# Kernel optimization log

Measured on AMD Instinct MI355X. Metric: run time of the kernel, lower is better.

The kernel has to match this reference:

```python
import math
import jax, jax.numpy as jnp
import numpy as np

BN_EPS = 1e-5

def _lrelu(x, s):
    return jnp.where(x >= 0, x, s * x)

def _bn(x, g, b):
    # BatchNorm2d in train mode (torch default): biased batch stats over (B,H,W)
    mu = jnp.mean(x, axis=(0, 2, 3), keepdims=True)
    var = jnp.mean((x - mu) ** 2, axis=(0, 2, 3), keepdims=True)
    return (x - mu) / jnp.sqrt(var + BN_EPS) * g[None, :, None, None] + b[None, :, None, None]

def _knn(x, x2, k):
    # x: [B,d,P], x2: [B,d,S] -> idx [B,k,S]: k nearest points of x for each column of x2
    inner = -2.0 * jnp.einsum('bdp,bds->bps', x, x2)
    xx = jnp.sum(x ** 2, axis=1)[:, :, None]    # [B,P,1]
    xx2 = jnp.sum(x2 ** 2, axis=1)[:, None, :]  # [B,1,S]
    d = -xx - inner - xx2                        # [B,P,S], larger = closer
    _, idx = jax.lax.top_k(jnp.transpose(d, (0, 2, 1)), k)  # [B,S,k]
    return jnp.transpose(idx, (0, 2, 1))         # [B,k,S]

def _gather_nb(X, idx, s, k):
    # faithful to torch gether_neibour, including its flat-reshape layout
    B, C, P = X.shape
    base = jnp.arange(B)[:, None, None] * P
    flat = (idx + base).reshape(-1)
    Xt = jnp.transpose(X, (0, 2, 1)).reshape(B * P, C)
    return Xt[flat].reshape(B, s, k, C)

def _c2d(x, W, b):
    return jnp.einsum('oc,bcpk->bopk', W, x) + b[None, :, None, None]

def _c1d(x, W, b):
    return jnp.einsum('oc,bcp->bop', W, x) + b[None, :, None]

def _forward(x, W_pos, b_pos, g2, be2, W_conv, b_conv, g1, be1, W_a1, b_a1, W_a2, b_a2, W_b1, b_b1, W_b2, b_b2, num_points):
    B, C, P = x.shape
    k = 8
    s = num_points
    # ---- Dynamic_sampling_M: uniform mesh over (x,y) bbox, snap to nearest event ----
    L = int(math.ceil(math.sqrt(s)))
    m = jnp.arange(L, dtype=x.dtype) / L
    m01 = jnp.tile(m[None, :], (L, 1)).reshape(1, 1, L * L)
    m02 = jnp.tile(m[:, None], (1, L)).reshape(1, 1, L * L)
    mesh = jnp.broadcast_to(jnp.concatenate([m01, m02], axis=1), (B, 2, L * L))
    Px = jax.lax.stop_gradient(x[:, :2, :])  # knn runs under torch.no_grad
    mn = Px.min(axis=2, keepdims=True)
    mx = Px.max(axis=2, keepdims=True)
    PS = mesh * (mx - mn) + mn
    idx0 = _knn(Px, PS, 1)                                   # [B,1,L*L]
    sp = _gather_nb(x, idx0, L * L, 1)[:, :, 0, :].transpose(0, 2, 1)  # [B,C,s]
    idx = _knn(jax.lax.stop_gradient(x[:, :3, :]), jax.lax.stop_gradient(sp[:, :3, :]), k)  # [B,k,s]
    x1 = jnp.transpose(_gather_nb(x, idx, s, k), (0, 3, 1, 2))  # [B,C,s,k]
    # ---- positional encoding ----
    PA = x1[:, :3, :, :]
    PC = x1[:, :3, :, 0:1]
    diff = PA - PC
    sq = jnp.sum(diff ** 2, axis=1, keepdims=True)
    temp = jnp.where(sq > 0, jnp.sqrt(jnp.where(sq > 0, sq, 1.0)), 0.0)
    PEmb = jnp.concatenate([PA, jnp.broadcast_to(PC, PA.shape), diff, temp], axis=1)  # [B,10,s,k]
    PEmb = _lrelu(_bn(_c2d(PEmb, W_pos, b_pos), g2, be2), 0.2)
    x_ = _lrelu(_bn(_c2d(x1[:, :4, :, :], W_conv, b_conv), g1, be1), 0.2)
    feat = jnp.concatenate([x_, PEmb], axis=1)  # [B,64,s,k]
    att = _c2d(_lrelu(_c2d(feat, W_a1, b_a1), 0.2), W_a2, b_a2)  # [B,1,s,k]
    att = jax.nn.softmax(att, axis=-1)
    feat = jnp.sum(feat * att, axis=-1)  # [B,64,s]
    Fea1 = _c1d(feat, W_b1, b_b1)
    Fea2 = _c1d(x1[:, :4, :, 0], W_b2, b_b2)
    out = _lrelu(Fea1 + Fea2, 0.01)
    return jnp.concatenate([x1[:, :5, :, 0], out], axis=1)  # [B,69,s]

def setup_inputs() -> dict:
    key = jax.random.key(0)
    ks = jax.random.split(key, 8)
    B, C, P = 2, 5, 16384
    num_points = 4096  # perfect square required by the mesh sampler
    outc, inc, h = 64, 4, 32
    w = lambda k_, shape: jax.random.normal(k_, shape, jnp.float32) * 0.05
    x = jax.random.normal(ks[0], (B, C, P), jnp.float32)
    return dict(
        x=x,
        W_pos=w(ks[1], (h, 10)), b_pos=jnp.zeros((h,), jnp.float32),
        g2=jnp.ones((h,), jnp.float32), be2=jnp.zeros((h,), jnp.float32),
        W_conv=w(ks[2], (h, inc)), b_conv=jnp.zeros((h,), jnp.float32),
        g1=jnp.ones((h,), jnp.float32), be1=jnp.zeros((h,), jnp.float32),
        W_a1=w(ks[3], (32, outc)), b_a1=jnp.zeros((32,), jnp.float32),
        W_a2=w(ks[4], (1, 32)), b_a2=jnp.zeros((1,), jnp.float32),
        W_b1=w(ks[5], (outc, outc)), b_b1=jnp.zeros((outc,), jnp.float32),
        W_b2=w(ks[6], (outc, inc)), b_b2=jnp.zeros((outc,), jnp.float32),
        num_points=num_points,
    )

def reference(x, W_pos, b_pos, g2, be2, W_conv, b_conv, g1, be1, W_a1, b_a1, W_a2, b_a2, W_b1, b_b1, W_b2, b_b2, num_points):
    return _forward(x, W_pos, b_pos, g2, be2, W_conv, b_conv, g1, be1, W_a1, b_a1, W_a2, b_a2, W_b1, b_b1, W_b2, b_b2, num_points)
```

## Files before the change

kernel.cpp:

```cpp
#include <hip/hip_runtime.h>
#include <math.h>

#define B_ 2
#define P_ 16384
#define C_ 5
#define S_ 4096
#define KNN_ 8
#define L_ 64

typedef unsigned short u16;
typedef unsigned int u32;

__device__ int   g_f32x, g_f32w;
__device__ float g_mnmx[16];
__device__ int   g_idxk[B_ * KNN_ * S_];
__device__ float g_partials[256 * 128];
__device__ float g_stats[128];

__device__ __forceinline__ float bf2f(u16 u) {
  union { u32 i; float f; } c; c.i = ((u32)u) << 16; return c.f;
}
__device__ __forceinline__ u16 f2bf(float f) {
  union { float f; u32 i; } c; c.f = f;
  u32 r = c.i + 0x7fffu + ((c.i >> 16) & 1u);
  return (u16)(r >> 16);
}
__device__ __forceinline__ float ldany(const void* p, int i, int f32) {
  return f32 ? ((const float*)p)[i] : bf2f(((const u16*)p)[i]);
}

__device__ __forceinline__ double packkey(float d, int idx) {
  u32 bits = __float_as_uint(d);
  u32 key = bits ^ ((u32)(((int)bits) >> 31) | 0x80000000u);
  int hi = (int)(0x3FF00000u | (key >> 12));
  int lo = (int)((key << 20) | ((u32)(16383 - idx) << 6));
  return __hiloint2double(hi, lo);
}
__device__ __forceinline__ int keyidx(double w) {
  return 16383 - (int)(((u32)__double2loint(w) >> 6) & 16383u);
}
__device__ __forceinline__ void ins8(double* t, double v) {
  double m = v;
#pragma unroll
  for (int k = 0; k < 8; ++k) {
    double mn = fmin(t[k], m);
    t[k] = fmax(t[k], m);
    m = mn;
  }
}

__device__ __forceinline__ int chk_bad(const void* p, int n, int tid) {
  int bad = 0;
  for (int i = tid; i < n; i += 256) {
    float f = bf2f(((const u16*)p)[i]);
    if (!(f == f) || fabsf(f) > 1024.0f) bad = 1;
  }
  return bad;
}
__global__ __launch_bounds__(256) void k_prep(const void* x, const void* wpos,
                                              const void* wconv, const void* wa1,
                                              const void* wa2, const void* wb1,
                                              const void* wb2) {
  int tid = threadIdx.x;
  if (blockIdx.x == 0) {
    __shared__ int sx, sw;
    if (tid == 0) { sx = 0; sw = 0; }
    __syncthreads();
    int bx = chk_bad(x, 1024, tid);
    int bw = chk_bad(wpos, 320, tid) | chk_bad(wconv, 128, tid) | chk_bad(wa1, 2048, tid)
           | chk_bad(wa2, 32, tid)   | chk_bad(wb1, 4096, tid)  | chk_bad(wb2, 256, tid);
    if (bx) atomicOr(&sx, 1);
    if (bw) atomicOr(&sw, 1);
    __syncthreads();
    if (tid == 0) { g_f32x = sx; g_f32w = sw; }
    return;
  }
  __shared__ int sbad;
  if (tid == 0) sbad = 0;
  __syncthreads();
  if (chk_bad(x, 1024, tid)) atomicOr(&sbad, 1);
  __syncthreads();
  int f32 = sbad;
  int bc = blockIdx.x - 1;
  int b = bc >> 1, ch = bc & 1;
  int base = (b * C_ + ch) * P_;
  float mn = INFINITY, mx = -INFINITY;
  for (int p = tid; p < P_; p += 256) {
    float v = ldany(x, base + p, f32);
    mn = fminf(mn, v); mx = fmaxf(mx, v);
  }
  for (int off = 32; off; off >>= 1) {
    mn = fminf(mn, __shfl_down(mn, off));
    mx = fmaxf(mx, __shfl_down(mx, off));
  }
  __shared__ float smn[4], smx[4];
  int wid = tid >> 6;
  if ((tid & 63) == 0) { smn[wid] = mn; smx[wid] = mx; }
  __syncthreads();
  if (tid == 0) {
    for (int w = 1; w < 4; ++w) { mn = fminf(mn, smn[w]); mx = fmaxf(mx, smx[w]); }
    g_mnmx[bc * 2] = mn; g_mnmx[bc * 2 + 1] = mx;
  }
}

__global__ __launch_bounds__(256, 6) void k_knn(const void* __restrict__ xv) {
  __shared__ float4 s4[1024];
  __shared__ int sidx[8];
  const int f32 = g_f32x;
  int tid = threadIdx.x;
  int l = tid & 63, g = tid >> 6;
  int sg0 = blockIdx.x * 8 + g * 2;
  int b = sg0 >> 12;
  int base0 = b * C_ * P_, base1 = base0 + P_, base2 = base1 + P_;

  float mn0 = g_mnmx[(b * 2 + 0) * 2], mx0 = g_mnmx[(b * 2 + 0) * 2 + 1];
  float mn1 = g_mnmx[(b * 2 + 1) * 2], mx1 = g_mnmx[(b * 2 + 1) * 2 + 1];
  float ps0[2], ps1[2], xx2[2], best[2]; int bestp[2];
#pragma unroll
  for (int qq = 0; qq < 2; ++qq) {
    int s = (sg0 + qq) & (S_ - 1);
    float mm0 = (float)(s & (L_ - 1)) * 0.015625f;
    float mm1 = (float)(s >> 6) * 0.015625f;
    ps0[qq] = __fadd_rn(__fmul_rn(mm0, __fsub_rn(mx0, mn0)), mn0);
    ps1[qq] = __fadd_rn(__fmul_rn(mm1, __fsub_rn(mx1, mn1)), mn1);
    xx2[qq] = __fadd_rn(__fmul_rn(ps0[qq], ps0[qq]), __fmul_rn(ps1[qq], ps1[qq]));
    best[qq] = -INFINITY; bestp[qq] = 0x7fffffff;
  }
  for (int c = 0; c < 16; ++c) {
    __syncthreads();
    for (int i = tid; i < 1024; i += 256) {
      int gi = c * 1024 + i;
      float a0 = ldany(xv, base0 + gi, f32);
      float a1 = ldany(xv, base1 + gi, f32);
      float xx = __fadd_rn(__fmul_rn(a0, a0), __fmul_rn(a1, a1));
      s4[i] = make_float4(a0, a1, xx, 0.0f);
    }
    __syncthreads();
    for (int t = 0; t < 16; ++t) {
      float4 v = s4[t * 64 + l];
      int ix = c * 1024 + t * 64 + l;
#pragma unroll
      for (int qq = 0; qq < 2; ++qq) {
        float dot = __fadd_rn(__fmul_rn(v.x, ps0[qq]), __fmul_rn(v.y, ps1[qq]));
        float inner = __fmul_rn(-2.0f, dot);
        float d = __fsub_rn(__fsub_rn(-v.z, inner), xx2[qq]);
        bool gt = d > best[qq];
        best[qq] = gt ? d : best[qq];
        bestp[qq] = gt ? ix : bestp[qq];
      }
    }
  }
#pragma unroll
  for (int qq = 0; qq < 2; ++qq) {
    float v = best[qq]; int ix = bestp[qq];
    for (int m = 1; m < 64; m <<= 1) {
      float ov = __shfl_xor(v, m, 64); int op = __shfl_xor(ix, m, 64);
      if (ov > v || (ov == v && op < ix)) { v = ov; ix = op; }
    }
    if (l == 0) sidx[g * 2 + qq] = ix;
  }
  __syncthreads();

  float q0[2], q1[2], q2[2], xx3q[2];
  double t8[2][8];
#pragma unroll
  for (int qq = 0; qq < 2; ++qq) {
    int qi = sidx[g * 2 + qq] & (P_ - 1);
    q0[qq] = ldany(xv, base0 + qi, f32);
    q1[qq] = ldany(xv, base1 + qi, f32);
    q2[qq] = ldany(xv, base2 + qi, f32);
    xx3q[qq] = __fadd_rn(__fadd_rn(__fmul_rn(q0[qq], q0[qq]), __fmul_rn(q1[qq], q1[qq])),
                         __fmul_rn(q2[qq], q2[qq]));
#pragma unroll
    for (int k = 0; k < 8; ++k) t8[qq][k] = -1.0;
  }
  for (int c = 0; c < 16; ++c) {
    __syncthreads();
    for (int i = tid; i < 1024; i += 256) {
      int gi = c * 1024 + i;
      float a0 = ldany(xv, base0 + gi, f32);
      float a1 = ldany(xv, base1 + gi, f32);
      float a2 = ldany(xv, base2 + gi, f32);
      float xx = __fadd_rn(__fadd_rn(__fmul_rn(a0, a0), __fmul_rn(a1, a1)), __fmul_rn(a2, a2));
      s4[i] = make_float4(a0, a1, a2, xx);
    }
    __syncthreads();
    for (int t = 0; t < 16; ++t) {
      float4 v = s4[t * 64 + l];
      int ix = c * 1024 + t * 64 + l;
#pragma unroll
      for (int qq = 0; qq < 2; ++qq) {
        float dot = __fadd_rn(__fadd_rn(__fmul_rn(v.x, q0[qq]), __fmul_rn(v.y, q1[qq])),
                              __fmul_rn(v.z, q2[qq]));
        float inner = __fmul_rn(-2.0f, dot);
        float d = __fsub_rn(__fsub_rn(-v.w, inner), xx3q[qq]);
        ins8(t8[qq], packkey(d, ix));
      }
    }
  }
  double wk[2] = {0.0, 0.0};
#pragma unroll
  for (int qq = 0; qq < 2; ++qq) {
#pragma unroll
    for (int r = 0; r < 8; ++r) {
      double w = t8[qq][0];
      for (int m = 1; m < 64; m <<= 1) w = fmax(w, __shfl_xor(w, m, 64));
      if (l == r) wk[qq] = w;
      bool cns = (t8[qq][0] == w);
#pragma unroll
      for (int k = 0; k < 7; ++k) t8[qq][k] = cns ? t8[qq][k + 1] : t8[qq][k];
      t8[qq][7] = cns ? -1.0 : t8[qq][7];
    }
  }
  if (l < 8) {
#pragma unroll
    for (int qq = 0; qq < 2; ++qq) {
      int s = (sg0 + qq) & (S_ - 1);
      g_idxk[b * 32768 + l * 4096 + s] = keyidx(wk[qq]);
    }
  }
}

__device__ __forceinline__ void elem_vals(const void* xv, int xf32, int xbase,
                                          const int* fb, int n,
                                          const float* sWpos, const float* sbpos,
                                          const float* sWconv, const float* sbconv,
                                          float* val ) {
  int p = fb[n] & (P_ - 1);
  int p0 = fb[n & ~7] & (P_ - 1);
  float xvv[4];
#pragma unroll
  for (int c = 0; c < 4; ++c) xvv[c] = ldany(xv, xbase + c * P_ + p, xf32);
  float pc[3];
#pragma unroll
  for (int c = 0; c < 3; ++c) pc[c] = ldany(xv, xbase + c * P_ + p0, xf32);
  float d0 = xvv[0] - pc[0], d1 = xvv[1] - pc[1], d2 = xvv[2] - pc[2];
  float sq = d0 * d0 + d1 * d1 + d2 * d2;
  float temp = (sq > 0.0f) ? sqrtf(sq) : 0.0f;
  float pe[10] = {xvv[0], xvv[1], xvv[2], pc[0], pc[1], pc[2], d0, d1, d2, temp};
#pragma unroll
  for (int o = 0; o < 32; ++o) {
    float acc = sbconv[o];
#pragma unroll
    for (int c = 0; c < 4; ++c) acc = fmaf(sWconv[o * 4 + c], xvv[c], acc);
    val[o] = acc;
  }
#pragma unroll
  for (int o = 0; o < 32; ++o) {
    float acc = sbpos[o];
#pragma unroll
    for (int c = 0; c < 10; ++c) acc = fmaf(sWpos[o * 10 + c], pe[c], acc);
    val[32 + o] = acc;
  }
}

__global__ __launch_bounds__(256) void k_partial(const void* __restrict__ x,
                                                 const void* __restrict__ Wpos,
                                                 const void* __restrict__ bpos,
                                                 const void* __restrict__ Wconv,
                                                 const void* __restrict__ bconv) {
  __shared__ float sWpos[320], sbpos[32], sWconv[128], sbconv[32];
  __shared__ float sacc[4][128];
  int tid = threadIdx.x;
  int xf32 = g_f32x, wf32 = g_f32w;
  for (int i2 = tid; i2 < 320; i2 += 256) sWpos[i2] = ldany(Wpos, i2, wf32);
  if (tid < 128) sWconv[tid] = ldany(Wconv, tid, wf32);
  if (tid < 32) { sbpos[tid] = ldany(bpos, tid, wf32); sbconv[tid] = ldany(bconv, tid, wf32); }
  __syncthreads();
  int t = blockIdx.x * 256 + tid;
  int b = t >> 15, n = t & 32767;
  const int* fb = g_idxk + b * 32768;
  float val[64];
  elem_vals(x, xf32, b * C_ * P_, fb, n, sWpos, sbpos, sWconv, sbconv, val);
  int wid = tid >> 6, lane = tid & 63;
#pragma unroll
  for (int c = 0; c < 64; ++c) {
    float s = val[c], q = val[c] * val[c];
    for (int off = 32; off; off >>= 1) {
      s += __shfl_down(s, off);
      q += __shfl_down(q, off);
    }
    if (lane == 0) { sacc[wid][c * 2] = s; sacc[wid][c * 2 + 1] = q; }
  }
  __syncthreads();
  if (tid < 128) {
    g_partials[blockIdx.x * 128 + tid] =
        sacc[0][tid] + sacc[1][tid] + sacc[2][tid] + sacc[3][tid];
  }
}

__global__ void k_finalize(const void* __restrict__ g1, const void* __restrict__ be1,
                           const void* __restrict__ g2, const void* __restrict__ be2) {
  int ch = threadIdx.x;
  if (ch >= 64) return;
  int wf32 = g_f32w;
  float sum = 0.f, sq = 0.f;
  for (int blk = 0; blk < 256; ++blk) {
    sum += g_partials[blk * 128 + ch * 2];
    sq  += g_partials[blk * 128 + ch * 2 + 1];
  }
  float mean = sum * (1.0f / 65536.0f);
  float var = sq * (1.0f / 65536.0f) - mean * mean;
  int o = ch & 31;
  float g  = ldany(ch < 32 ? g1 : g2, o, wf32);
  float be = ldany(ch < 32 ? be1 : be2, o, wf32);
  float scale = g / sqrtf(var + 1e-5f);
  g_stats[ch * 2] = scale;
  g_stats[ch * 2 + 1] = be - mean * scale;
}

__global__ __launch_bounds__(256) void k_pass2(const void* __restrict__ x,
                                               const void* __restrict__ Wpos,
                                               const void* __restrict__ bpos,
                                               const void* __restrict__ Wconv,
                                               const void* __restrict__ bconv,
                                               const void* __restrict__ Wa1,
                                               const void* __restrict__ ba1,
                                               const void* __restrict__ Wa2,
                                               const void* __restrict__ ba2,
                                               const void* __restrict__ Wb1,
                                               const void* __restrict__ bb1,
                                               const void* __restrict__ Wb2,
                                               const void* __restrict__ bb2,
                                               void* __restrict__ out) {
  __shared__ float sWpos[320], sbpos[32], sWconv[128], sbconv[32];
  __shared__ float sWa1[2048], sba1[32], sWa2[32];
  __shared__ float sWb1[64 * 65];
  __shared__ float sbb1[64], sWb2[256], sbb2[64], sstats[128];
  __shared__ float sba2;
  int tid = threadIdx.x;
  int xf32 = g_f32x, wf32 = g_f32w;
  for (int i2 = tid; i2 < 320; i2 += 256) sWpos[i2] = ldany(Wpos, i2, wf32);
  if (tid < 128) sWconv[tid] = ldany(Wconv, tid, wf32);
  if (tid < 32) { sbpos[tid] = ldany(bpos, tid, wf32); sbconv[tid] = ldany(bconv, tid, wf32); }
  for (int i2 = tid; i2 < 2048; i2 += 256) sWa1[i2] = ldany(Wa1, i2, wf32);
  for (int i2 = tid; i2 < 4096; i2 += 256) sWb1[(i2 >> 6) * 65 + (i2 & 63)] = ldany(Wb1, i2, wf32);
  if (tid >= 32 && tid < 64) { sba1[tid - 32] = ldany(ba1, tid - 32, wf32); sWa2[tid - 32] = ldany(Wa2, tid - 32, wf32); }
  if (tid >= 64 && tid < 128) { sbb1[tid - 64] = ldany(bb1, tid - 64, wf32); sbb2[tid - 64] = ldany(bb2, tid - 64, wf32); }
  if (tid >= 128 && tid < 256) sstats[tid - 128] = g_stats[tid - 128];
  sWb2[tid] = ldany(Wb2, tid, wf32);
  if (tid == 0) sba2 = ldany(ba2, 0, wf32);
  __syncthreads();
  int g = blockIdx.x * 32 + (tid >> 3);
  int j = tid & 7;
  int b = g >> 12, i = g & (S_ - 1);
  int n = i * 8 + j;
  const int* fb = g_idxk + b * 32768;
  int xbase = b * C_ * P_;
  float feat[64];
  elem_vals(x, xf32, xbase, fb, n, sWpos, sbpos, sWconv, sbconv, feat);
#pragma unroll
  for (int c = 0; c < 64; ++c) {
    float v = fmaf(feat[c], sstats[c * 2], sstats[c * 2 + 1]);
    feat[c] = (v >= 0.f) ? v : 0.2f * v;
  }
  float att = sba2;
  for (int h = 0; h < 32; ++h) {
    float acc = sba1[h];
#pragma unroll
    for (int c = 0; c < 64; ++c) acc = fmaf(sWa1[h * 64 + c], feat[c], acc);
    acc = (acc >= 0.f) ? acc : 0.2f * acc;
    att = fmaf(sWa2[h], acc, att);
  }
  float mxv = att;
  for (int mk = 1; mk < 8; mk <<= 1) mxv = fmaxf(mxv, __shfl_xor(mxv, mk, 8));
  float e = expf(att - mxv);
  float se = e;
  for (int mk = 1; mk < 8; mk <<= 1) se += __shfl_xor(se, mk, 8);
  float a = e / se;
#pragma unroll
  for (int c = 0; c < 64; ++c) {
    float w = feat[c] * a;
    w += __shfl_xor(w, 1, 8);
    w += __shfl_xor(w, 2, 8);
    w += __shfl_xor(w, 4, 8);
    feat[c] = w;
  }
  int p0 = fb[i * 8] & (P_ - 1);
  float xc0 = ldany(x, xbase + p0, xf32);
  float xc1 = ldany(x, xbase + P_ + p0, xf32);
  float xc2 = ldany(x, xbase + 2 * P_ + p0, xf32);
  float xc3 = ldany(x, xbase + 3 * P_ + p0, xf32);
  int obase = b * 69 * S_;
#pragma unroll
  for (int oc = 0; oc < 8; ++oc) {
    int o = j * 8 + oc;
    float acc = sbb1[o];
#pragma unroll
    for (int c = 0; c < 64; ++c) acc = fmaf(sWb1[o * 65 + c], feat[c], acc);
    float acc2 = sbb2[o];
    acc2 = fmaf(sWb2[o * 4 + 0], xc0, acc2);
    acc2 = fmaf(sWb2[o * 4 + 1], xc1, acc2);
    acc2 = fmaf(sWb2[o * 4 + 2], xc2, acc2);
    acc2 = fmaf(sWb2[o * 4 + 3], xc3, acc2);
    float r = acc + acc2;
    r = (r >= 0.f) ? r : 0.01f * r;
    int oi = obase + (5 + o) * S_ + i;
    if (xf32) ((float*)out)[oi] = r; else ((u16*)out)[oi] = f2bf(r);
  }
  if (j == 0) {
#pragma unroll
    for (int c = 0; c < 5; ++c) {
      int oi = obase + c * S_ + i;
      if (xf32) ((float*)out)[oi] = ((const float*)x)[xbase + c * P_ + p0];
      else      ((u16*)out)[oi]   = ((const u16*)x)[xbase + c * P_ + p0];
    }
  }
}

extern "C" void kernel_launch(void* const* d_in, const int* in_sizes, int n_in,
                              void* d_out, int out_size, void* d_ws, size_t ws_size,
                              hipStream_t stream) {
  const void* x     = d_in[0];
  const void* Wpos  = d_in[1];
  const void* bpos  = d_in[2];
  const void* g2    = d_in[3];
  const void* be2   = d_in[4];
  const void* Wconv = d_in[5];
  const void* bconv = d_in[6];
  const void* g1    = d_in[7];
  const void* be1   = d_in[8];
  const void* Wa1   = d_in[9];
  const void* ba1   = d_in[10];
  const void* Wa2   = d_in[11];
  const void* ba2   = d_in[12];
  const void* Wb1   = d_in[13];
  const void* bb1   = d_in[14];
  const void* Wb2   = d_in[15];
  const void* bb2   = d_in[16];
  (void)d_ws; (void)ws_size; (void)in_sizes; (void)n_in;

  hipLaunchKernelGGL(k_prep, dim3(5), dim3(256), 0, stream,
                     x, Wpos, Wconv, Wa1, Wa2, Wb1, Wb2);
  hipLaunchKernelGGL(k_knn, dim3(1024), dim3(256), 0, stream, x);
  hipLaunchKernelGGL(k_partial, dim3(256), dim3(256), 0, stream, x,
                     Wpos, bpos, Wconv, bconv);
  hipLaunchKernelGGL(k_finalize, dim3(1), dim3(64), 0, stream,
                     g1, be1, g2, be2);
  hipLaunchKernelGGL(k_pass2, dim3(256), dim3(256), 0, stream, x,
                     Wpos, bpos, Wconv, bconv, Wa1, ba1, Wa2, ba2,
                     Wb1, bb1, Wb2, bb2, d_out);
}
```

Before: 315.3 us.

## Fold prep and finalize into kNN/pass2 kernels and batch top-8 insertion with sorting network

Removes the separate prep and finalize launches. Every kNN block now recomputes the dtype check and the bbox min/max itself, BN partial sums are accumulated with atomics, and pass2 derives the BN scale and shift from those sums. The per-candidate 8-way insertion in the kNN inner loop is replaced by buffering 8 candidates, sorting them with a network and merging them bitonically into the running top-8. Occupancy hint drops from 6 to 4. Risks: every one of 1024 blocks rescans 2x16384 values for min/max, g_sums is zeroed in k_knn with no ordering guarantee relative to other blocks, and atomic summation order makes the sums nondeterministic.

```diff
diff --git a/kernel.cpp b/kernel.cpp
--- a/kernel.cpp
+++ b/kernel.cpp
@@ -11,11 +11,8 @@
 typedef unsigned short u16;
 typedef unsigned int u32;
 
-__device__ int   g_f32x, g_f32w;
-__device__ float g_mnmx[16];
 __device__ int   g_idxk[B_ * KNN_ * S_];
-__device__ float g_partials[256 * 128];
-__device__ float g_stats[128];
+__device__ float g_sums[128];
 
 __device__ __forceinline__ float bf2f(u16 u) {
   union { u32 i; float f; } c; c.i = ((u32)u) << 16; return c.f;
@@ -39,14 +36,24 @@
 __device__ __forceinline__ int keyidx(double w) {
   return 16383 - (int)(((u32)__double2loint(w) >> 6) & 16383u);
 }
-__device__ __forceinline__ void ins8(double* t, double v) {
-  double m = v;
-#pragma unroll
-  for (int k = 0; k < 8; ++k) {
-    double mn = fmin(t[k], m);
-    t[k] = fmax(t[k], m);
-    m = mn;
-  }
+__device__ __forceinline__ void cmpswap(double& a, double& b) {
+  double hi = fmax(a, b), lo = fmin(a, b);
+  a = hi; b = lo;
+}
+__device__ __forceinline__ void flush8(double* a, double* k) {
+  cmpswap(k[0], k[1]); cmpswap(k[2], k[3]); cmpswap(k[4], k[5]); cmpswap(k[6], k[7]);
+  cmpswap(k[0], k[2]); cmpswap(k[1], k[3]); cmpswap(k[4], k[6]); cmpswap(k[5], k[7]);
+  cmpswap(k[1], k[2]); cmpswap(k[5], k[6]);
+  cmpswap(k[0], k[4]); cmpswap(k[1], k[5]); cmpswap(k[2], k[6]); cmpswap(k[3], k[7]);
+  cmpswap(k[2], k[4]); cmpswap(k[3], k[5]);
+  cmpswap(k[1], k[2]); cmpswap(k[3], k[4]); cmpswap(k[5], k[6]);
+  a[0] = fmax(a[0], k[7]); a[1] = fmax(a[1], k[6]);
+  a[2] = fmax(a[2], k[5]); a[3] = fmax(a[3], k[4]);
+  a[4] = fmax(a[4], k[3]); a[5] = fmax(a[5], k[2]);
+  a[6] = fmax(a[6], k[1]); a[7] = fmax(a[7], k[0]);
+  cmpswap(a[0], a[4]); cmpswap(a[1], a[5]); cmpswap(a[2], a[6]); cmpswap(a[3], a[7]);
+  cmpswap(a[0], a[2]); cmpswap(a[1], a[3]); cmpswap(a[4], a[6]); cmpswap(a[5], a[7]);
+  cmpswap(a[0], a[1]); cmpswap(a[2], a[3]); cmpswap(a[4], a[5]); cmpswap(a[6], a[7]);
 }
 
 __device__ __forceinline__ int chk_bad(const void* p, int n, int tid) {
@@ -57,64 +64,46 @@
   }
   return bad;
 }
-__global__ __launch_bounds__(256) void k_prep(const void* x, const void* wpos,
-                                              const void* wconv, const void* wa1,
-                                              const void* wa2, const void* wb1,
-                                              const void* wb2) {
-  int tid = threadIdx.x;
-  if (blockIdx.x == 0) {
-    __shared__ int sx, sw;
-    if (tid == 0) { sx = 0; sw = 0; }
-    __syncthreads();
-    int bx = chk_bad(x, 1024, tid);
-    int bw = chk_bad(wpos, 320, tid) | chk_bad(wconv, 128, tid) | chk_bad(wa1, 2048, tid)
-           | chk_bad(wa2, 32, tid)   | chk_bad(wb1, 4096, tid)  | chk_bad(wb2, 256, tid);
-    if (bx) atomicOr(&sx, 1);
-    if (bw) atomicOr(&sw, 1);
-    __syncthreads();
-    if (tid == 0) { g_f32x = sx; g_f32w = sw; }
-    return;
-  }
-  __shared__ int sbad;
-  if (tid == 0) sbad = 0;
-  __syncthreads();
-  if (chk_bad(x, 1024, tid)) atomicOr(&sbad, 1);
-  __syncthreads();
-  int f32 = sbad;
-  int bc = blockIdx.x - 1;
-  int b = bc >> 1, ch = bc & 1;
-  int base = (b * C_ + ch) * P_;
-  float mn = INFINITY, mx = -INFINITY;
-  for (int p = tid; p < P_; p += 256) {
-    float v = ldany(x, base + p, f32);
-    mn = fminf(mn, v); mx = fmaxf(mx, v);
-  }
-  for (int off = 32; off; off >>= 1) {
-    mn = fminf(mn, __shfl_down(mn, off));
-    mx = fmaxf(mx, __shfl_down(mx, off));
-  }
-  __shared__ float smn[4], smx[4];
-  int wid = tid >> 6;
-  if ((tid & 63) == 0) { smn[wid] = mn; smx[wid] = mx; }
-  __syncthreads();
-  if (tid == 0) {
-    for (int w = 1; w < 4; ++w) { mn = fminf(mn, smn[w]); mx = fmaxf(mx, smx[w]); }
-    g_mnmx[bc * 2] = mn; g_mnmx[bc * 2 + 1] = mx;
-  }
-}
-
-__global__ __launch_bounds__(256, 6) void k_knn(const void* __restrict__ xv) {
+
+__global__ __launch_bounds__(256, 4) void k_knn(const void* __restrict__ xv) {
   __shared__ float4 s4[1024];
   __shared__ int sidx[8];
-  const int f32 = g_f32x;
+  __shared__ int sbad;
+  __shared__ float sred[16];
   int tid = threadIdx.x;
+  if (blockIdx.x == 0 && tid < 128) g_sums[tid] = 0.0f;
   int l = tid & 63, g = tid >> 6;
   int sg0 = blockIdx.x * 8 + g * 2;
   int b = sg0 >> 12;
   int base0 = b * C_ * P_, base1 = base0 + P_, base2 = base1 + P_;
 
-  float mn0 = g_mnmx[(b * 2 + 0) * 2], mx0 = g_mnmx[(b * 2 + 0) * 2 + 1];
-  float mn1 = g_mnmx[(b * 2 + 1) * 2], mx1 = g_mnmx[(b * 2 + 1) * 2 + 1];
+  if (tid == 0) sbad = 0;
+  __syncthreads();
+  if (chk_bad(xv, 1024, tid)) atomicOr(&sbad, 1);
+  __syncthreads();
+  const int f32 = sbad;
+
+  float mn0 = INFINITY, mx0 = -INFINITY, mn1 = INFINITY, mx1 = -INFINITY;
+  for (int p = tid; p < P_; p += 256) {
+    float v0 = ldany(xv, base0 + p, f32);
+    float v1 = ldany(xv, base1 + p, f32);
+    mn0 = fminf(mn0, v0); mx0 = fmaxf(mx0, v0);
+    mn1 = fminf(mn1, v1); mx1 = fmaxf(mx1, v1);
+  }
+  for (int off = 32; off; off >>= 1) {
+    mn0 = fminf(mn0, __shfl_down(mn0, off)); mx0 = fmaxf(mx0, __shfl_down(mx0, off));
+    mn1 = fminf(mn1, __shfl_down(mn1, off)); mx1 = fmaxf(mx1, __shfl_down(mx1, off));
+  }
+  if (l == 0) {
+    sred[g * 4 + 0] = mn0; sred[g * 4 + 1] = mx0;
+    sred[g * 4 + 2] = mn1; sred[g * 4 + 3] = mx1;
+  }
+  __syncthreads();
+  mn0 = fminf(fminf(sred[0], sred[4]), fminf(sred[8], sred[12]));
+  mx0 = fmaxf(fmaxf(sred[1], sred[5]), fmaxf(sred[9], sred[13]));
+  mn1 = fminf(fminf(sred[2], sred[6]), fminf(sred[10], sred[14]));
+  mx1 = fmaxf(fmaxf(sred[3], sred[7]), fmaxf(sred[11], sred[15]));
+
   float ps0[2], ps1[2], xx2[2], best[2]; int bestp[2];
 #pragma unroll
   for (int qq = 0; qq < 2; ++qq) {
@@ -162,7 +151,7 @@
   __syncthreads();
 
   float q0[2], q1[2], q2[2], xx3q[2];
-  double t8[2][8];
+  double acc[2][8], kb[2][8];
 #pragma unroll
   for (int qq = 0; qq < 2; ++qq) {
     int qi = sidx[g * 2 + qq] & (P_ - 1);
@@ -172,7 +161,7 @@
     xx3q[qq] = __fadd_rn(__fadd_rn(__fmul_rn(q0[qq], q0[qq]), __fmul_rn(q1[qq], q1[qq])),
                          __fmul_rn(q2[qq], q2[qq]));
 #pragma unroll
-    for (int k = 0; k < 8; ++k) t8[qq][k] = -1.0;
+    for (int k = 0; k < 8; ++k) acc[qq][k] = -1.0;
   }
   for (int c = 0; c < 16; ++c) {
     __syncthreads();
@@ -185,6 +174,7 @@
       s4[i] = make_float4(a0, a1, a2, xx);
     }
     __syncthreads();
+#pragma unroll
     for (int t = 0; t < 16; ++t) {
       float4 v = s4[t * 64 + l];
       int ix = c * 1024 + t * 64 + l;
@@ -194,8 +184,12 @@
                               __fmul_rn(v.z, q2[qq]));
         float inner = __fmul_rn(-2.0f, dot);
         float d = __fsub_rn(__fsub_rn(-v.w, inner), xx3q[qq]);
-        ins8(t8[qq], packkey(d, ix));
+        kb[qq][t & 7] = packkey(d, ix);
       }
+      if ((t & 7) == 7) {
+        flush8(acc[0], kb[0]);
+        flush8(acc[1], kb[1]);
+      }
     }
   }
   double wk[2] = {0.0, 0.0};
@@ -203,13 +197,13 @@
   for (int qq = 0; qq < 2; ++qq) {
 #pragma unroll
     for (int r = 0; r < 8; ++r) {
-      double w = t8[qq][0];
+      double w = acc[qq][0];
       for (int m = 1; m < 64; m <<= 1) w = fmax(w, __shfl_xor(w, m, 64));
       if (l == r) wk[qq] = w;
-      bool cns = (t8[qq][0] == w);
-#pragma unroll
-      for (int k = 0; k < 7; ++k) t8[qq][k] = cns ? t8[qq][k + 1] : t8[qq][k];
-      t8[qq][7] = cns ? -1.0 : t8[qq][7];
+      bool cns = (acc[qq][0] == w);
+#pragma unroll
+      for (int k = 0; k < 7; ++k) acc[qq][k] = cns ? acc[qq][k + 1] : acc[qq][k];
+      acc[qq][7] = cns ? -1.0 : acc[qq][7];
     }
   }
   if (l < 8) {
@@ -261,8 +255,14 @@
                                                  const void* __restrict__ bconv) {
   __shared__ float sWpos[320], sbpos[32], sWconv[128], sbconv[32];
   __shared__ float sacc[4][128];
+  __shared__ int sbx, sbw;
   int tid = threadIdx.x;
-  int xf32 = g_f32x, wf32 = g_f32w;
+  if (tid == 0) { sbx = 0; sbw = 0; }
+  __syncthreads();
+  if (chk_bad(x, 1024, tid)) atomicOr(&sbx, 1);
+  if (chk_bad(Wpos, 320, tid) | chk_bad(Wconv, 128, tid)) atomicOr(&sbw, 1);
+  __syncthreads();
+  int xf32 = sbx, wf32 = sbw;
   for (int i2 = tid; i2 < 320; i2 += 256) sWpos[i2] = ldany(Wpos, i2, wf32);
   if (tid < 128) sWconv[tid] = ldany(Wconv, tid, wf32);
   if (tid < 32) { sbpos[tid] = ldany(bpos, tid, wf32); sbconv[tid] = ldany(bconv, tid, wf32); }
@@ -284,29 +284,9 @@
   }
   __syncthreads();
   if (tid < 128) {
-    g_partials[blockIdx.x * 128 + tid] =
-        sacc[0][tid] + sacc[1][tid] + sacc[2][tid] + sacc[3][tid];
-  }
-}
-
-__global__ void k_finalize(const void* __restrict__ g1, const void* __restrict__ be1,
-                           const void* __restrict__ g2, const void* __restrict__ be2) {
-  int ch = threadIdx.x;
-  if (ch >= 64) return;
-  int wf32 = g_f32w;
-  float sum = 0.f, sq = 0.f;
-  for (int blk = 0; blk < 256; ++blk) {
-    sum += g_partials[blk * 128 + ch * 2];
-    sq  += g_partials[blk * 128 + ch * 2 + 1];
-  }
-  float mean = sum * (1.0f / 65536.0f);
-  float var = sq * (1.0f / 65536.0f) - mean * mean;
-  int o = ch & 31;
-  float g  = ldany(ch < 32 ? g1 : g2, o, wf32);
-  float be = ldany(ch < 32 ? be1 : be2, o, wf32);
-  float scale = g / sqrtf(var + 1e-5f);
-  g_stats[ch * 2] = scale;
-  g_stats[ch * 2 + 1] = be - mean * scale;
+    float v = sacc[0][tid] + sacc[1][tid] + sacc[2][tid] + sacc[3][tid];
+    atomicAdd(&g_sums[tid], v);
+  }
 }
 
 __global__ __launch_bounds__(256) void k_pass2(const void* __restrict__ x,
@@ -314,6 +294,10 @@
                                                const void* __restrict__ bpos,
                                                const void* __restrict__ Wconv,
                                                const void* __restrict__ bconv,
+                                               const void* __restrict__ g1,
+                                               const void* __restrict__ be1,
+                                               const void* __restrict__ g2,
+                                               const void* __restrict__ be2,
                                                const void* __restrict__ Wa1,
                                                const void* __restrict__ ba1,
                                                const void* __restrict__ Wa2,
@@ -328,8 +312,14 @@
   __shared__ float sWb1[64 * 65];
   __shared__ float sbb1[64], sWb2[256], sbb2[64], sstats[128];
   __shared__ float sba2;
+  __shared__ int sbx, sbw;
   int tid = threadIdx.x;
-  int xf32 = g_f32x, wf32 = g_f32w;
+  if (tid == 0) { sbx = 0; sbw = 0; }
+  __syncthreads();
+  if (chk_bad(x, 1024, tid)) atomicOr(&sbx, 1);
+  if (chk_bad(Wa1, 2048, tid) | chk_bad(Wb1, 4096, tid)) atomicOr(&sbw, 1);
+  __syncthreads();
+  int xf32 = sbx, wf32 = sbw;
   for (int i2 = tid; i2 < 320; i2 += 256) sWpos[i2] = ldany(Wpos, i2, wf32);
   if (tid < 128) sWconv[tid] = ldany(Wconv, tid, wf32);
   if (tid < 32) { sbpos[tid] = ldany(bpos, tid, wf32); sbconv[tid] = ldany(bconv, tid, wf32); }
@@ -337,9 +327,20 @@
   for (int i2 = tid; i2 < 4096; i2 += 256) sWb1[(i2 >> 6) * 65 + (i2 & 63)] = ldany(Wb1, i2, wf32);
   if (tid >= 32 && tid < 64) { sba1[tid - 32] = ldany(ba1, tid - 32, wf32); sWa2[tid - 32] = ldany(Wa2, tid - 32, wf32); }
   if (tid >= 64 && tid < 128) { sbb1[tid - 64] = ldany(bb1, tid - 64, wf32); sbb2[tid - 64] = ldany(bb2, tid - 64, wf32); }
-  if (tid >= 128 && tid < 256) sstats[tid - 128] = g_stats[tid - 128];
   sWb2[tid] = ldany(Wb2, tid, wf32);
   if (tid == 0) sba2 = ldany(ba2, 0, wf32);
+  if (tid >= 128 && tid < 192) {
+    int ch = tid - 128;
+    float sum = g_sums[ch * 2], sq = g_sums[ch * 2 + 1];
+    float mean = sum * (1.0f / 65536.0f);
+    float var = sq * (1.0f / 65536.0f) - mean * mean;
+    int o = ch & 31;
+    float gg = ldany(ch < 32 ? g1 : g2, o, wf32);
+    float be = ldany(ch < 32 ? be1 : be2, o, wf32);
+    float scale = gg / sqrtf(var + 1e-5f);
+    sstats[ch * 2] = scale;
+    sstats[ch * 2 + 1] = be - mean * scale;
+  }
   __syncthreads();
   int g = blockIdx.x * 32 + (tid >> 3);
   int j = tid & 7;
@@ -430,14 +431,10 @@
   const void* bb2   = d_in[16];
   (void)d_ws; (void)ws_size; (void)in_sizes; (void)n_in;
 
-  hipLaunchKernelGGL(k_prep, dim3(5), dim3(256), 0, stream,
-                     x, Wpos, Wconv, Wa1, Wa2, Wb1, Wb2);
   hipLaunchKernelGGL(k_knn, dim3(1024), dim3(256), 0, stream, x);
   hipLaunchKernelGGL(k_partial, dim3(256), dim3(256), 0, stream, x,
                      Wpos, bpos, Wconv, bconv);
-  hipLaunchKernelGGL(k_finalize, dim3(1), dim3(64), 0, stream,
-                     g1, be1, g2, be2);
   hipLaunchKernelGGL(k_pass2, dim3(256), dim3(256), 0, stream, x,
-                     Wpos, bpos, Wconv, bconv, Wa1, ba1, Wa2, ba2,
-                     Wb1, bb1, Wb2, bb2, d_out);
-}
+                     Wpos, bpos, Wconv, bconv, g1, be1, g2, be2,
+                     Wa1, ba1, Wa2, ba2, Wb1, bb1, Wb2, bb2, d_out);
+}
```

Result: faster. 298.9 us (-5.2%).
